# Kernel optimization log

Measured on AMD Instinct MI355X. Metric: run time of the kernel, lower is better.

Reference implementation:

```python
import jax, jax.numpy as jnp
import numpy as np

EMBED_DIM = 1024
NUM_HEADS = 16
HEAD_DIM = EMBED_DIM // NUM_HEADS
BATCH, SEQ = 1, 4096


def setup_inputs() -> dict:
    key = jax.random.key(0)
    ks = jax.random.split(key, 9)
    s = 1.0 / np.sqrt(EMBED_DIM)
    x = jax.random.normal(ks[0], (BATCH, SEQ, EMBED_DIM), dtype=jnp.float32)
    def lin(kw, kb):
        W = jax.random.uniform(kw, (EMBED_DIM, EMBED_DIM), jnp.float32, -s, s)
        b = jax.random.uniform(kb, (EMBED_DIM,), jnp.float32, -s, s)
        return W, b
    Wq, bq = lin(ks[1], ks[2])
    Wk, bk = lin(ks[3], ks[4])
    Wv, bv = lin(ks[5], ks[6])
    Wo, bo = lin(ks[7], ks[8])
    return {"x": x, "Wq": Wq, "bq": bq, "Wk": Wk, "bk": bk,
            "Wv": Wv, "bv": bv, "Wo": Wo, "bo": bo}


def _split_heads(t):  # [B,S,E] -> [B,H,S,D]
    B, S, _ = t.shape
    return t.reshape(B, S, NUM_HEADS, HEAD_DIM).transpose(0, 2, 1, 3)


def reference(x, Wq, bq, Wk, bk, Wv, bv, Wo, bo):
    scale = HEAD_DIM ** -0.5
    q = _split_heads(x @ Wq.T + bq)
    k = _split_heads(x @ Wk.T + bk)
    v = _split_heads(x @ Wv.T + bv)
    # explicit attention matrix, as in the torch module
    scores = jnp.einsum('bhqd,bhkd->bhqk', q * scale, k)
    weights = jax.nn.softmax(scores, axis=-1)
    out = jnp.einsum('bhqk,bhkd->bhqd', weights, v)
    B, H, S, D = out.shape
    out = out.transpose(0, 2, 1, 3).reshape(B, S, H * D)
    return out @ Wo.T + bo
```

## Files before the change

### kernel.cpp

```cpp
#include <hip/hip_runtime.h>


typedef unsigned short u16;
using bf16x8 = __attribute__((ext_vector_type(8))) __bf16;
using bf16x4 = __attribute__((ext_vector_type(4))) __bf16;
using f32x4  = __attribute__((ext_vector_type(4))) float;

__device__ __forceinline__ u16 f2bf(float f) {
  unsigned u = __float_as_uint(f);
  u += 0x7fffu + ((u >> 16) & 1u);
  return (u16)(u >> 16);
}
__device__ __forceinline__ float bf2f(u16 h) {
  return __uint_as_float(((unsigned)h) << 16);
}
__device__ __forceinline__ float fexp2(float x) {
  return __builtin_amdgcn_exp2f(x);
}

#define GLOAD16(gptr, lptr)                                                   \
  __builtin_amdgcn_global_load_lds(                                           \
      (const __attribute__((address_space(1))) unsigned int*)(gptr),          \
      (__attribute__((address_space(3))) unsigned int*)(lptr), 16, 0, 0)

__device__ __forceinline__ f32x4 mfma16(bf16x8 a, bf16x8 b, f32x4 c) {
  return __builtin_amdgcn_mfma_f32_16x16x32_bf16(a, b, c, 0, 0, 0);
}

__device__ __forceinline__ bf16x8 lds_read8(const u16* base, int row, int col) {
  int boff = (row * 128 + col * 2) ^ ((row & 7) << 4);
  return *(const bf16x8*)((const char*)base + boff);
}

__global__ void cvt_all(const float* __restrict__ x, const float* __restrict__ Wq,
                        const float* __restrict__ Wk, const float* __restrict__ Wv,
                        const float* __restrict__ Wo, u16* __restrict__ xb,
                        u16* __restrict__ Wqb, u16* __restrict__ Wkb,
                        u16* __restrict__ Wvb, u16* __restrict__ Woh,
                        u16* __restrict__ Wol) {
  int b = blockIdx.x;
  if (b < 7168) {
    const float* src; u16* dst; int base;
    if (b < 4096)      { src = x;  dst = xb;  base = b; }
    else if (b < 5120) { src = Wq; dst = Wqb; base = b - 4096; }
    else if (b < 6144) { src = Wk; dst = Wkb; base = b - 5120; }
    else               { src = Wv; dst = Wvb; base = b - 6144; }
    int i = base * 256 + threadIdx.x;
    float4 v = ((const float4*)src)[i];
    ushort4 o;
    o.x = f2bf(v.x); o.y = f2bf(v.y); o.z = f2bf(v.z); o.w = f2bf(v.w);
    ((ushort4*)dst)[i] = o;
  } else {
    int i = (b - 7168) * 256 + threadIdx.x;
    float4 v = ((const float4*)Wo)[i];
    ushort4 h, l;
    h.x = f2bf(v.x); l.x = f2bf(v.x - bf2f(h.x));
    h.y = f2bf(v.y); l.y = f2bf(v.y - bf2f(h.y));
    h.z = f2bf(v.z); l.z = f2bf(v.z - bf2f(h.z));
    h.w = f2bf(v.w); l.w = f2bf(v.w - bf2f(h.w));
    ((ushort4*)Woh)[i] = h;
    ((ushort4*)Wol)[i] = l;
  }
}

struct GemmMat {
  const u16* Bh;
  const float* bias;
  u16* oh;
  u16* ovt;
  float scale;
};
struct GemmParams {
  const u16* Ah;
  GemmMat mm[3];
};

__global__ __launch_bounds__(256, 2) void gemm_qkv(GemmParams p) {
  const int tid = threadIdx.x;
  const int lane = tid & 63, w = tid >> 6;
  const int wr = w >> 1, wc = w & 1;
  const int lg = lane >> 4, lr = lane & 15;
  const GemmMat g = p.mm[blockIdx.z];
  const int brow = blockIdx.y, bcol = blockIdx.x;

  __shared__ u16 As[128 * 64];
  __shared__ u16 Bs[128 * 64];

  f32x4 acc[4][4];
#pragma unroll
  for (int m = 0; m < 4; ++m)
#pragma unroll
    for (int n = 0; n < 4; ++n) acc[m][n] = f32x4{0.f, 0.f, 0.f, 0.f};

  for (int k0 = 0; k0 < 1024; k0 += 64) {
#pragma unroll
    for (int it = 0; it < 4; ++it) {
      int c = tid + it * 256;
      int row = c >> 3, cc = c & 7;
      int scc = cc ^ (row & 7);
      size_t ga = (size_t)(brow * 128 + row) * 1024 + k0 + scc * 8;
      size_t gb = (size_t)(bcol * 128 + row) * 1024 + k0 + scc * 8;
      GLOAD16(p.Ah + ga, &As[c * 8]);
      GLOAD16(g.Bh + gb, &Bs[c * 8]);
    }
    __syncthreads();

    bf16x8 a[4][2], b[4][2];
#pragma unroll
    for (int m = 0; m < 4; ++m)
#pragma unroll
      for (int kk = 0; kk < 2; ++kk)
        a[m][kk] = lds_read8(As, 64 * wr + 16 * m + lr, 32 * kk + 8 * lg);
#pragma unroll
    for (int n = 0; n < 4; ++n)
#pragma unroll
      for (int kk = 0; kk < 2; ++kk)
        b[n][kk] = lds_read8(Bs, 64 * wc + 16 * n + lr, 32 * kk + 8 * lg);
#pragma unroll
    for (int m = 0; m < 4; ++m)
#pragma unroll
      for (int n = 0; n < 4; ++n) {
        acc[m][n] = mfma16(a[m][0], b[n][0], acc[m][n]);
        acc[m][n] = mfma16(a[m][1], b[n][1], acc[m][n]);
      }
    __syncthreads();
  }

#pragma unroll
  for (int n = 0; n < 4; ++n) {
    int gcol = bcol * 128 + 64 * wc + 16 * n + lr;
    float bs = g.bias[gcol];
#pragma unroll
    for (int m = 0; m < 4; ++m) {
      int grow0 = brow * 128 + 64 * wr + 16 * m + 4 * lg;
      float v0 = (acc[m][n][0] + bs) * g.scale;
      float v1 = (acc[m][n][1] + bs) * g.scale;
      float v2 = (acc[m][n][2] + bs) * g.scale;
      float v3 = (acc[m][n][3] + bs) * g.scale;
      if (g.ovt) {
        ushort4 hs;
        hs.x = f2bf(v0); hs.y = f2bf(v1); hs.z = f2bf(v2); hs.w = f2bf(v3);
        *(ushort4*)&g.ovt[(size_t)gcol * 4096 + grow0] = hs;
      } else {
        g.oh[(size_t)(grow0 + 0) * 1024 + gcol] = f2bf(v0);
        g.oh[(size_t)(grow0 + 1) * 1024 + gcol] = f2bf(v1);
        g.oh[(size_t)(grow0 + 2) * 1024 + gcol] = f2bf(v2);
        g.oh[(size_t)(grow0 + 3) * 1024 + gcol] = f2bf(v3);
      }
    }
  }
}

__global__ __launch_bounds__(256, 2) void gemm_out64(
    const u16* __restrict__ Ah, const u16* __restrict__ Al,
    const u16* __restrict__ Bh, const u16* __restrict__ Bl,
    const float* __restrict__ bias, float* __restrict__ out) {
  const int tid = threadIdx.x;
  const int lane = tid & 63, w = tid >> 6;
  const int lg = lane >> 4, lr = lane & 15;
  const int brow = blockIdx.y, bcol = blockIdx.x;

  __shared__ u16 As[2][64 * 32];
  __shared__ u16 Bs[2][128 * 32];

  f32x4 acc[4][2];
#pragma unroll
  for (int m = 0; m < 4; ++m)
#pragma unroll
    for (int n = 0; n < 2; ++n) acc[m][n] = f32x4{0.f, 0.f, 0.f, 0.f};

  for (int k0 = 0; k0 < 1024; k0 += 32) {
    {
      int c = tid;
      int row = c >> 2, cc = c & 3;
      size_t ga = (size_t)(brow * 64 + row) * 1024 + k0 + cc * 8;
      GLOAD16(Ah + ga, &As[0][c * 8]);
      GLOAD16(Al + ga, &As[1][c * 8]);
    }
#pragma unroll
    for (int it = 0; it < 2; ++it) {
      int c = tid + it * 256;
      int row = c >> 2, cc = c & 3;
      size_t gb = (size_t)(bcol * 128 + row) * 1024 + k0 + cc * 8;
      GLOAD16(Bh + gb, &Bs[0][c * 8]);
      GLOAD16(Bl + gb, &Bs[1][c * 8]);
    }
    __syncthreads();

    bf16x8 a[4], a2[4], b[2], b2[2];
#pragma unroll
    for (int m = 0; m < 4; ++m) {
      int off = (16 * m + lr) * 32 + 8 * lg;
      a[m]  = *(const bf16x8*)&As[0][off];
      a2[m] = *(const bf16x8*)&As[1][off];
    }
#pragma unroll
    for (int n = 0; n < 2; ++n) {
      int off = (32 * w + 16 * n + lr) * 32 + 8 * lg;
      b[n]  = *(const bf16x8*)&Bs[0][off];
      b2[n] = *(const bf16x8*)&Bs[1][off];
    }
#pragma unroll
    for (int m = 0; m < 4; ++m)
#pragma unroll
      for (int n = 0; n < 2; ++n) {
        acc[m][n] = mfma16(a[m], b[n], acc[m][n]);
        acc[m][n] = mfma16(a[m], b2[n], acc[m][n]);
        acc[m][n] = mfma16(a2[m], b[n], acc[m][n]);
      }
    __syncthreads();
  }

#pragma unroll
  for (int n = 0; n < 2; ++n) {
    int gcol = bcol * 128 + 32 * w + 16 * n + lr;
    float bs = bias[gcol];
#pragma unroll
    for (int m = 0; m < 4; ++m) {
      int grow0 = brow * 64 + 16 * m + 4 * lg;
#pragma unroll
      for (int j = 0; j < 4; ++j)
        out[(size_t)(grow0 + j) * 1024 + gcol] = acc[m][n][j] + bs;
    }
  }
}

__global__ __launch_bounds__(256, 2) void attn_kernel(
    const u16* __restrict__ Qb, const u16* __restrict__ Kb,
    const u16* __restrict__ Vt, u16* __restrict__ ctxh,
    u16* __restrict__ ctxl) {
  const int tid = threadIdx.x;
  const int lane = tid & 63, w = tid >> 6;
  const int lg = lane >> 4, lr = lane & 15;
  const int hd = blockIdx.x;
  const int q0 = blockIdx.y * 128;

  __shared__ u16 Ks[2][64 * 64];
  __shared__ u16 Vs[3][64 * 64];
  __shared__ u16 Ps[4][2][2][16 * 64];

  bf16x8 qf[2][2];
#pragma unroll
  for (int qs = 0; qs < 2; ++qs) {
    size_t qbase = (size_t)(q0 + 32 * w + 16 * qs + lr) * 1024 + hd * 64;
    qf[qs][0] = *(const bf16x8*)&Qb[qbase + 8 * lg];
    qf[qs][1] = *(const bf16x8*)&Qb[qbase + 32 + 8 * lg];
  }

  bf16x8 ones;
#pragma unroll
  for (int i = 0; i < 8; ++i) ones[i] = (__bf16)1.0f;

  f32x4 o[2][4], lacc[2];
#pragma unroll
  for (int qs = 0; qs < 2; ++qs) {
    lacc[qs] = f32x4{0.f, 0.f, 0.f, 0.f};
#pragma unroll
    for (int n = 0; n < 4; ++n) o[qs][n] = f32x4{0.f, 0.f, 0.f, 0.f};
  }

  auto stageK = [&](int buf, int kv0) {
#pragma unroll
    for (int it = 0; it < 2; ++it) {
      int c = tid + it * 256;
      int kv = c >> 3, cc = c & 7;
      int scc = cc ^ (kv & 7);
      GLOAD16(Kb + (size_t)(kv0 + kv) * 1024 + hd * 64 + scc * 8,
              &Ks[buf][c * 8]);
    }
  };
  auto stageV = [&](int buf, int kv0) {
#pragma unroll
    for (int it = 0; it < 2; ++it) {
      int c = tid + it * 256;
      int d = c >> 3, cc = c & 7;
      int scc = cc ^ (d & 7);
      GLOAD16(Vt + (size_t)(hd * 64 + d) * 4096 + kv0 + scc * 8,
              &Vs[buf][c * 8]);
    }
  };

  auto pv = [&](int vbuf, int ph) {
    __builtin_amdgcn_s_setprio(1);
#pragma unroll
    for (int ks = 0; ks < 2; ++ks) {
      bf16x8 pf0 = lds_read8(&Ps[w][ph][0][0], lr, 32 * ks + 8 * lg);
      bf16x8 pf1 = lds_read8(&Ps[w][ph][1][0], lr, 32 * ks + 8 * lg);
      lacc[0] = mfma16(ones, pf0, lacc[0]);
      lacc[1] = mfma16(ones, pf1, lacc[1]);
#pragma unroll
      for (int nb = 0; nb < 4; ++nb) {
        bf16x8 vf = lds_read8(&Vs[vbuf][0], 16 * nb + lr, 32 * ks + 8 * lg);
        o[0][nb] = mfma16(vf, pf0, o[0][nb]);
        o[1][nb] = mfma16(vf, pf1, o[1][nb]);
      }
    }
    __builtin_amdgcn_s_setprio(0);
  };

  stageK(0, 0);
  stageV(0, 0);

  int vprev = 2, vcur = 0, vnext = 1;

  for (int t = 0; t < 64; ++t) {
    if (t < 63) {
      stageK((t + 1) & 1, (t + 1) * 64);
      stageV(vnext, (t + 1) * 64);
      asm volatile("s_waitcnt vmcnt(4)" ::: "memory");
    } else {
      asm volatile("s_waitcnt vmcnt(0)" ::: "memory");
    }
    asm volatile("s_waitcnt lgkmcnt(0)" ::: "memory");
    __builtin_amdgcn_s_barrier();

    f32x4 s[2][4];
#pragma unroll
    for (int qs = 0; qs < 2; ++qs)
#pragma unroll
      for (int nb = 0; nb < 4; ++nb) s[qs][nb] = f32x4{0.f, 0.f, 0.f, 0.f};
    const u16* kbase = &Ks[t & 1][0];
    __builtin_amdgcn_s_setprio(1);
#pragma unroll
    for (int nb = 0; nb < 4; ++nb)
#pragma unroll
      for (int ks = 0; ks < 2; ++ks) {
        bf16x8 kf = lds_read8(kbase, 16 * nb + lr, 32 * ks + 8 * lg);
        s[0][nb] = mfma16(kf, qf[0][ks], s[0][nb]);
        s[1][nb] = mfma16(kf, qf[1][ks], s[1][nb]);
      }
    __builtin_amdgcn_s_setprio(0);

    if (t > 0) pv(vprev, (t - 1) & 1);

#pragma unroll
    for (int qs = 0; qs < 2; ++qs)
#pragma unroll
      for (int nb = 0; nb < 4; ++nb) {
        bf16x4 pk;
        pk[0] = (__bf16)fexp2(s[qs][nb][0]);
        pk[1] = (__bf16)fexp2(s[qs][nb][1]);
        pk[2] = (__bf16)fexp2(s[qs][nb][2]);
        pk[3] = (__bf16)fexp2(s[qs][nb][3]);
        int boff = (lr * 128 + (16 * nb + 4 * lg) * 2) ^ ((lr & 7) << 4);
        *(bf16x4*)((char*)&Ps[w][t & 1][qs][0] + boff) = pk;
      }

    int tmp = vprev; vprev = vcur; vcur = vnext; vnext = tmp;
  }

  pv(vprev, 1);

#pragma unroll
  for (int qs = 0; qs < 2; ++qs) {
    const float linv = 1.0f / lacc[qs][0];
    const size_t grow = (size_t)(q0 + 32 * w + 16 * qs + lr) * 1024;
#pragma unroll
    for (int nb = 0; nb < 4; ++nb) {
      ushort4 hs, ls;
      float v0 = o[qs][nb][0] * linv, v1 = o[qs][nb][1] * linv;
      float v2 = o[qs][nb][2] * linv, v3 = o[qs][nb][3] * linv;
      hs.x = f2bf(v0); ls.x = f2bf(v0 - bf2f(hs.x));
      hs.y = f2bf(v1); ls.y = f2bf(v1 - bf2f(hs.y));
      hs.z = f2bf(v2); ls.z = f2bf(v2 - bf2f(hs.z));
      hs.w = f2bf(v3); ls.w = f2bf(v3 - bf2f(hs.w));
      size_t gc = grow + hd * 64 + 16 * nb + 4 * lg;
      *(ushort4*)&ctxh[gc] = hs;
      *(ushort4*)&ctxl[gc] = ls;
    }
  }
}

extern "C" void kernel_launch(void* const* d_in, const int* in_sizes, int n_in,
                              void* d_out, int out_size, void* d_ws,
                              size_t ws_size, hipStream_t stream) {
  const float* x  = (const float*)d_in[0];
  const float* Wq = (const float*)d_in[1];
  const float* bq = (const float*)d_in[2];
  const float* Wk = (const float*)d_in[3];
  const float* bk = (const float*)d_in[4];
  const float* Wv = (const float*)d_in[5];
  const float* bv = (const float*)d_in[6];
  const float* Wo = (const float*)d_in[7];
  const float* bo = (const float*)d_in[8];

  const size_t M1 = 1024u * 1024u;
  u16* p = (u16*)d_ws;
  u16* xb   = p + 0;
  u16* Qb   = p + 4 * M1;
  u16* Kb   = p + 8 * M1;
  u16* ctxl = p + 12 * M1;
  u16* Vtb  = p + 16 * M1;
  u16* Wqb  = p + 20 * M1;
  u16* Wkb  = p + 21 * M1;
  u16* Wvb  = p + 22 * M1;
  u16* Woh  = p + 23 * M1;
  u16* Wol  = p + 24 * M1;
  u16* ctxh = xb;

  cvt_all<<<8192, 256, 0, stream>>>(x, Wq, Wk, Wv, Wo, xb, Wqb, Wkb, Wvb, Woh,
                                    Wol);

  GemmParams pq;
  pq.Ah = xb;
  pq.mm[0] = {Wqb, bq, Qb, nullptr, 0.125f * 1.44269504f};
  pq.mm[1] = {Wkb, bk, Kb, nullptr, 1.0f};
  pq.mm[2] = {Wvb, bv, nullptr, Vtb, 1.0f};
  gemm_qkv<<<dim3(8, 32, 3), 256, 0, stream>>>(pq);

  attn_kernel<<<dim3(16, 32), 256, 0, stream>>>(Qb, Kb, Vtb, ctxh, ctxl);

  gemm_out64<<<dim3(8, 64), 256, 0, stream>>>(ctxh, ctxl, Woh, Wol, bo,
                                              (float*)d_out);
}
```

Before: 163.5 us.

## Halve attention block size and drop deferred PV software pipeline

The attention kernel now runs 128-thread blocks covering 64 query rows, which doubles the grid to 1024 blocks and shrinks per-block shared memory. The one-iteration-delayed PV step with triple-buffered V is replaced by double-buffered K/V and an in-iteration PV using a single P buffer, followed by a trailing barrier. The aim is more blocks per CU and lower LDS use. In exchange it gives up the overlap between QK^T and PV and adds a second barrier per iteration. Each block also has to load every K/V tile for only half as many queries, doubling global K/V traffic.

```diff
diff --git a/kernel.cpp b/kernel.cpp
--- a/kernel.cpp
+++ b/kernel.cpp
@@ -225,7 +225,7 @@
   }
 }
 
-__global__ __launch_bounds__(256, 2) void attn_kernel(
+__global__ __launch_bounds__(128, 2) void attn_kernel(
     const u16* __restrict__ Qb, const u16* __restrict__ Kb,
     const u16* __restrict__ Vt, u16* __restrict__ ctxh,
     u16* __restrict__ ctxl) {
@@ -233,11 +233,11 @@
   const int lane = tid & 63, w = tid >> 6;
   const int lg = lane >> 4, lr = lane & 15;
   const int hd = blockIdx.x;
-  const int q0 = blockIdx.y * 128;
+  const int q0 = blockIdx.y * 64;
 
   __shared__ u16 Ks[2][64 * 64];
-  __shared__ u16 Vs[3][64 * 64];
-  __shared__ u16 Ps[4][2][2][16 * 64];
+  __shared__ u16 Vs[2][64 * 64];
+  __shared__ u16 Ps[2][2][16 * 64];
 
   bf16x8 qf[2][2];
 #pragma unroll
@@ -259,20 +259,18 @@
     for (int n = 0; n < 4; ++n) o[qs][n] = f32x4{0.f, 0.f, 0.f, 0.f};
   }
 
-  auto stageK = [&](int buf, int kv0) {
-#pragma unroll
-    for (int it = 0; it < 2; ++it) {
-      int c = tid + it * 256;
+  auto stage = [&](int buf, int kv0) {
+#pragma unroll
+    for (int it = 0; it < 4; ++it) {
+      int c = tid + it * 128;
       int kv = c >> 3, cc = c & 7;
       int scc = cc ^ (kv & 7);
       GLOAD16(Kb + (size_t)(kv0 + kv) * 1024 + hd * 64 + scc * 8,
               &Ks[buf][c * 8]);
     }
-  };
-  auto stageV = [&](int buf, int kv0) {
-#pragma unroll
-    for (int it = 0; it < 2; ++it) {
-      int c = tid + it * 256;
+#pragma unroll
+    for (int it = 0; it < 4; ++it) {
+      int c = tid + it * 128;
       int d = c >> 3, cc = c & 7;
       int scc = cc ^ (d & 7);
       GLOAD16(Vt + (size_t)(hd * 64 + d) * 4096 + kv0 + scc * 8,
@@ -280,38 +278,16 @@
     }
   };
 
-  auto pv = [&](int vbuf, int ph) {
-    __builtin_amdgcn_s_setprio(1);
-#pragma unroll
-    for (int ks = 0; ks < 2; ++ks) {
-      bf16x8 pf0 = lds_read8(&Ps[w][ph][0][0], lr, 32 * ks + 8 * lg);
-      bf16x8 pf1 = lds_read8(&Ps[w][ph][1][0], lr, 32 * ks + 8 * lg);
-      lacc[0] = mfma16(ones, pf0, lacc[0]);
-      lacc[1] = mfma16(ones, pf1, lacc[1]);
-#pragma unroll
-      for (int nb = 0; nb < 4; ++nb) {
-        bf16x8 vf = lds_read8(&Vs[vbuf][0], 16 * nb + lr, 32 * ks + 8 * lg);
-        o[0][nb] = mfma16(vf, pf0, o[0][nb]);
-        o[1][nb] = mfma16(vf, pf1, o[1][nb]);
-      }
-    }
-    __builtin_amdgcn_s_setprio(0);
-  };
-
-  stageK(0, 0);
-  stageV(0, 0);
-
-  int vprev = 2, vcur = 0, vnext = 1;
+  stage(0, 0);
 
   for (int t = 0; t < 64; ++t) {
+    const int cur = t & 1;
     if (t < 63) {
-      stageK((t + 1) & 1, (t + 1) * 64);
-      stageV(vnext, (t + 1) * 64);
-      asm volatile("s_waitcnt vmcnt(4)" ::: "memory");
+      stage(cur ^ 1, (t + 1) * 64);
+      asm volatile("s_waitcnt vmcnt(8)" ::: "memory");
     } else {
       asm volatile("s_waitcnt vmcnt(0)" ::: "memory");
     }
-    asm volatile("s_waitcnt lgkmcnt(0)" ::: "memory");
     __builtin_amdgcn_s_barrier();
 
     f32x4 s[2][4];
@@ -319,19 +295,16 @@
     for (int qs = 0; qs < 2; ++qs)
 #pragma unroll
       for (int nb = 0; nb < 4; ++nb) s[qs][nb] = f32x4{0.f, 0.f, 0.f, 0.f};
-    const u16* kbase = &Ks[t & 1][0];
     __builtin_amdgcn_s_setprio(1);
 #pragma unroll
     for (int nb = 0; nb < 4; ++nb)
 #pragma unroll
       for (int ks = 0; ks < 2; ++ks) {
-        bf16x8 kf = lds_read8(kbase, 16 * nb + lr, 32 * ks + 8 * lg);
+        bf16x8 kf = lds_read8(&Ks[cur][0], 16 * nb + lr, 32 * ks + 8 * lg);
         s[0][nb] = mfma16(kf, qf[0][ks], s[0][nb]);
         s[1][nb] = mfma16(kf, qf[1][ks], s[1][nb]);
       }
     __builtin_amdgcn_s_setprio(0);
-
-    if (t > 0) pv(vprev, (t - 1) & 1);
 
 #pragma unroll
     for (int qs = 0; qs < 2; ++qs)
@@ -343,13 +316,27 @@
         pk[2] = (__bf16)fexp2(s[qs][nb][2]);
         pk[3] = (__bf16)fexp2(s[qs][nb][3]);
         int boff = (lr * 128 + (16 * nb + 4 * lg) * 2) ^ ((lr & 7) << 4);
-        *(bf16x4*)((char*)&Ps[w][t & 1][qs][0] + boff) = pk;
-      }
-
-    int tmp = vprev; vprev = vcur; vcur = vnext; vnext = tmp;
-  }
-
-  pv(vprev, 1);
+        *(bf16x4*)((char*)&Ps[w][qs][0] + boff) = pk;
+      }
+
+    __builtin_amdgcn_s_setprio(1);
+#pragma unroll
+    for (int ks = 0; ks < 2; ++ks) {
+      bf16x8 pf0 = lds_read8(&Ps[w][0][0], lr, 32 * ks + 8 * lg);
+      bf16x8 pf1 = lds_read8(&Ps[w][1][0], lr, 32 * ks + 8 * lg);
+      lacc[0] = mfma16(ones, pf0, lacc[0]);
+      lacc[1] = mfma16(ones, pf1, lacc[1]);
+#pragma unroll
+      for (int nb = 0; nb < 4; ++nb) {
+        bf16x8 vf = lds_read8(&Vs[cur][0], 16 * nb + lr, 32 * ks + 8 * lg);
+        o[0][nb] = mfma16(vf, pf0, o[0][nb]);
+        o[1][nb] = mfma16(vf, pf1, o[1][nb]);
+      }
+    }
+    __builtin_amdgcn_s_setprio(0);
+
+    __builtin_amdgcn_s_barrier();
+  }
 
 #pragma unroll
   for (int qs = 0; qs < 2; ++qs) {
@@ -408,7 +395,7 @@
   pq.mm[2] = {Wvb, bv, nullptr, Vtb, 1.0f};
   gemm_qkv<<<dim3(8, 32, 3), 256, 0, stream>>>(pq);
 
-  attn_kernel<<<dim3(16, 32), 256, 0, stream>>>(Qb, Kb, Vtb, ctxh, ctxl);
+  attn_kernel<<<dim3(16, 64), 128, 0, stream>>>(Qb, Kb, Vtb, ctxh, ctxl);
 
   gemm_out64<<<dim3(8, 64), 256, 0, stream>>>(ctxh, ctxl, Woh, Wol, bo,
                                               (float*)d_out);
```

Result: slower. 176.2 us (+7.8%).
